# Kernel tuning notes

Hardware: AMD Instinct MI355X
Metric: run time of the kernel (lower is better)

Reference implementation:

```python
import jax, jax.numpy as jnp
import numpy as np

B, S, D, H = 2, 2048, 1024, 16
HD = D // H
SCALE = float(np.sqrt(HD))


def setup_inputs() -> dict:
    key = jax.random.key(0)
    ks = jax.random.split(key, 11)
    std = 1.0 / np.sqrt(D)
    inp = {
        "query": jax.random.normal(ks[0], (B, S, D), dtype=jnp.float32),
        "key": jax.random.normal(ks[1], (B, S, D), dtype=jnp.float32),
        "value": jax.random.normal(ks[2], (B, S, D), dtype=jnp.float32),
        "w_q": jax.random.normal(ks[3], (D, D), dtype=jnp.float32) * std,
        "b_q": jax.random.normal(ks[4], (D,), dtype=jnp.float32) * std,
        "w_k": jax.random.normal(ks[5], (D, D), dtype=jnp.float32) * std,
        "b_k": jax.random.normal(ks[6], (D,), dtype=jnp.float32) * std,
        "w_v": jax.random.normal(ks[7], (D, D), dtype=jnp.float32) * std,
        "b_v": jax.random.normal(ks[8], (D,), dtype=jnp.float32) * std,
        "w_fc": jax.random.normal(ks[9], (D, D), dtype=jnp.float32) * std,
        "b_fc": jax.random.normal(ks[10], (D,), dtype=jnp.float32) * std,
    }
    return inp


def reference(query, key, value, w_q, b_q, w_k, b_k, w_v, b_v, w_fc, b_fc):
    # Linear projections (torch Linear: x @ W^T + b; here w_* stored as [in, out])
    Q = query @ w_q + b_q            # [B, S, D]
    K = key @ w_k + b_k
    V = value @ w_v + b_v
    # split heads -> [B, H, S, HD]
    Q = Q.reshape(B, S, H, HD).transpose(0, 2, 1, 3)
    K = K.reshape(B, S, H, HD).transpose(0, 2, 1, 3)
    V = V.reshape(B, S, H, HD).transpose(0, 2, 1, 3)
    energy = jnp.einsum('bhqd,bhkd->bhqk', Q, K) / SCALE  # [B, H, S, S]
    attn = jax.nn.softmax(energy, axis=-1)
    x = jnp.einsum('bhqk,bhkd->bhqd', attn, V)            # [B, H, S, HD]
    x = x.transpose(0, 2, 1, 3).reshape(B, S, D)
    return x @ w_fc + b_fc
```

## Files before the change

### kernel.cpp

```cpp
#include <hip/hip_runtime.h>
#include <stdint.h>

#define Bz 2
#define Sz 2048
#define Dz 1024
#define Hz 16
#define HDz 64
#define Mz (Bz*Sz)

typedef unsigned short u16;
typedef __attribute__((ext_vector_type(8))) __bf16 bf16x8;
typedef __attribute__((ext_vector_type(8))) unsigned short u16x8;
typedef __attribute__((ext_vector_type(4))) float f32x4;

#define C1 0.1803368801111243f

__device__ __forceinline__ u16 f2bf(float f) {
  union { float f; unsigned u; } v; v.f = f;
  unsigned r = v.u + 0x7fffu + ((v.u >> 16) & 1u);
  return (u16)(r >> 16);
}

__device__ __forceinline__ void async16(void* lds, const void* g) {
  __builtin_amdgcn_global_load_lds(
      (const __attribute__((address_space(1))) unsigned int*)g,
      (__attribute__((address_space(3))) unsigned int*)lds, 16, 0, 0);
}

__global__ void cvt3_kernel(const float* __restrict__ q, const float* __restrict__ k,
                            const float* __restrict__ v,
                            u16* __restrict__ xq, u16* __restrict__ xk, u16* __restrict__ xv,
                            int n4) {
  const float* in = blockIdx.y == 0 ? q : blockIdx.y == 1 ? k : v;
  u16* out = blockIdx.y == 0 ? xq : blockIdx.y == 1 ? xk : xv;
  int i = blockIdx.x * blockDim.x + threadIdx.x;
  if (i < n4) {
    float4 t = ((const float4*)in)[i];
    ((ushort4*)out)[i] = make_ushort4(f2bf(t.x), f2bf(t.y), f2bf(t.z), f2bf(t.w));
  }
}

__global__ void wt_cvt_kernel(const float* __restrict__ w0, const float* __restrict__ w1,
                              const float* __restrict__ w2, const float* __restrict__ w3,
                              u16* __restrict__ Wt ) {
  const float* W = blockIdx.z == 0 ? w0 : blockIdx.z == 1 ? w1 : blockIdx.z == 2 ? w2 : w3;
  u16* o = Wt + (size_t)blockIdx.z * Dz * Dz;
  __shared__ __align__(16) float t[32][33];
  int n0 = blockIdx.x * 32, k0 = blockIdx.y * 32;
  int x = threadIdx.x, y = threadIdx.y;
#pragma unroll
  for (int i = 0; i < 4; ++i)
    t[y + i*8][x] = W[(size_t)(k0 + y + i*8) * Dz + n0 + x];
  __syncthreads();
#pragma unroll
  for (int i = 0; i < 4; ++i)
    o[(size_t)(n0 + y + i*8) * Dz + k0 + x] = f2bf(t[x][y + i*8]);
}

__global__ void __launch_bounds__(256)
vtrans_kernel(const u16* __restrict__ Vp, u16* __restrict__ Vt) {
  __shared__ __align__(16) u16 t[64][72];
  int s0 = blockIdx.x * 64, bh = blockIdx.y;
  int b = bh >> 4;
  int h = bh & 15;
  int tid = threadIdx.x;
#pragma unroll
  for (int p = 0; p < 4; ++p) {
    int c = p * 256 + tid;
    int row = c >> 4, off = (c & 15) * 4;
    ushort4 v = *(const ushort4*)(Vp + (size_t)(b * Sz + s0 + row) * Dz + h * 64 + off);
    *(ushort4*)&t[row][off] = v;
  }
  __syncthreads();
#pragma unroll
  for (int p = 0; p < 4; ++p) {
    int c = p * 256 + tid;
    int d = c >> 4, sc = (c & 15) * 4;
    ushort4 v = make_ushort4(t[sc + 0][d], t[sc + 1][d], t[sc + 2][d], t[sc + 3][d]);
    *(ushort4*)(Vt + (size_t)(bh * 64 + d) * Sz + s0 + sc) = v;
  }
}

__global__ void __launch_bounds__(256)
gemm_qkv(const u16* __restrict__ xq, const u16* __restrict__ xk, const u16* __restrict__ xv,
         const u16* __restrict__ Wt3,
         const float* __restrict__ bq, const float* __restrict__ bk, const float* __restrict__ bv,
         u16* __restrict__ Qp, u16* __restrict__ Kp, u16* __restrict__ Vp)
{
  __shared__ __align__(16) u16 lA[128][32];
  __shared__ __align__(16) u16 lB[128][32];
  const int sel = blockIdx.x >> 3;
  const int n0 = (blockIdx.x & 7) * 128;
  const int m0 = blockIdx.y * 128;
  const u16* A = sel == 0 ? xq : sel == 1 ? xk : xv;
  const u16* Bt = Wt3 + (size_t)sel * Dz * Dz;
  const float* bias = sel == 0 ? bq : sel == 1 ? bk : bv;
  u16* Cv = sel == 0 ? Qp : sel == 1 ? Kp : Vp;

  const int tid = threadIdx.x;
  const int w = tid >> 6, lane = tid & 63;
  const int wm = (w >> 1) * 64, wn = (w & 1) * 64;
  const int l16 = lane & 15, qd = lane >> 4;

  f32x4 acc[4][4];
#pragma unroll
  for (int i = 0; i < 4; ++i)
#pragma unroll
    for (int j = 0; j < 4; ++j) acc[i][j] = (f32x4){0.f, 0.f, 0.f, 0.f};

  const int r0 = tid >> 2, c0 = (tid & 3) * 8;
  const int r1 = r0 + 64;

  for (int k0 = 0; k0 < Dz; k0 += 32) {
    __syncthreads();
    async16(&lA[r0][c0], A  + (size_t)(m0 + r0) * Dz + k0 + c0);
    async16(&lB[r0][c0], Bt + (size_t)(n0 + r0) * Dz + k0 + c0);
    async16(&lA[r1][c0], A  + (size_t)(m0 + r1) * Dz + k0 + c0);
    async16(&lB[r1][c0], Bt + (size_t)(n0 + r1) * Dz + k0 + c0);
    __syncthreads();
    bf16x8 af[4], bfv[4];
#pragma unroll
    for (int t = 0; t < 4; ++t) {
      af[t]  = *(const bf16x8*)&lA[wm + t * 16 + l16][qd * 8];
      bfv[t] = *(const bf16x8*)&lB[wn + t * 16 + l16][qd * 8];
    }
#pragma unroll
    for (int mt = 0; mt < 4; ++mt)
#pragma unroll
      for (int nt = 0; nt < 4; ++nt)
        acc[mt][nt] = __builtin_amdgcn_mfma_f32_16x16x32_bf16(af[mt], bfv[nt], acc[mt][nt], 0, 0, 0);
  }

#pragma unroll
  for (int nt = 0; nt < 4; ++nt) {
    const int n = n0 + wn + nt * 16 + l16;
    const float bvl = bias[n];
#pragma unroll
    for (int mt = 0; mt < 4; ++mt)
#pragma unroll
      for (int r = 0; r < 4; ++r) {
        const int m = m0 + wm + mt * 16 + qd * 4 + r;
        Cv[(size_t)m * Dz + n] = f2bf(acc[mt][nt][r] + bvl);
      }
  }
}

__global__ void __launch_bounds__(256)
gemm_fc(const u16* __restrict__ A, const u16* __restrict__ Bt,
        const float* __restrict__ bias, float* __restrict__ C)
{
  __shared__ __align__(16) u16 lA[128][32];
  __shared__ __align__(16) u16 lB[64][32];
  const int m0 = blockIdx.y * 128, n0 = blockIdx.x * 64;
  const int tid = threadIdx.x;
  const int w = tid >> 6, lane = tid & 63;
  const int wm = (w >> 1) * 64, wn = (w & 1) * 32;
  const int l16 = lane & 15, qd = lane >> 4;

  f32x4 acc[4][2];
#pragma unroll
  for (int i = 0; i < 4; ++i)
#pragma unroll
    for (int j = 0; j < 2; ++j) acc[i][j] = (f32x4){0.f, 0.f, 0.f, 0.f};

  const int r0 = tid >> 2, c0 = (tid & 3) * 8;

  for (int k0 = 0; k0 < Dz; k0 += 32) {
    __syncthreads();
    async16(&lA[r0][c0],      A  + (size_t)(m0 + r0) * Dz + k0 + c0);
    async16(&lA[r0 + 64][c0], A  + (size_t)(m0 + r0 + 64) * Dz + k0 + c0);
    async16(&lB[r0][c0],      Bt + (size_t)(n0 + r0) * Dz + k0 + c0);
    __syncthreads();
    bf16x8 af[4], bfv[2];
#pragma unroll
    for (int t = 0; t < 4; ++t)
      af[t] = *(const bf16x8*)&lA[wm + t * 16 + l16][qd * 8];
#pragma unroll
    for (int t = 0; t < 2; ++t)
      bfv[t] = *(const bf16x8*)&lB[wn + t * 16 + l16][qd * 8];
#pragma unroll
    for (int mt = 0; mt < 4; ++mt)
#pragma unroll
      for (int nt = 0; nt < 2; ++nt)
        acc[mt][nt] = __builtin_amdgcn_mfma_f32_16x16x32_bf16(af[mt], bfv[nt], acc[mt][nt], 0, 0, 0);
  }

#pragma unroll
  for (int nt = 0; nt < 2; ++nt) {
    const int n = n0 + wn + nt * 16 + l16;
    const float bvl = bias[n];
#pragma unroll
    for (int mt = 0; mt < 4; ++mt)
#pragma unroll
      for (int r = 0; r < 4; ++r) {
        const int m = m0 + wm + mt * 16 + qd * 4 + r;
        C[(size_t)m * Dz + n] = acc[mt][nt][r] + bvl;
      }
  }
}

__global__ void __launch_bounds__(256, 2)
attn_kernel(const u16* __restrict__ Qp, const u16* __restrict__ Kp,
            const u16* __restrict__ Vt, u16* __restrict__ Ao)
{
  __shared__ __align__(16) u16 lK[128][72];
  __shared__ __align__(16) u16 lV[64][136];
  __shared__ __align__(16) u16 lP[4][32][136];

  const int q0 = blockIdx.x * 128;
  const int bh = blockIdx.y;
  const int b = bh >> 4, h = bh & 15;
  const int tid = threadIdx.x, w = tid >> 6, lane = tid & 63;
  const int l16 = lane & 15, qd = lane >> 4;

  const int krow = tid >> 3, kcol = (tid & 7) * 8;
  const int vrow = tid >> 4, vcol = (tid & 15) * 8;

  u16x8 kreg[4], vreg[4];
#pragma unroll
  for (int p = 0; p < 4; ++p) {
    kreg[p] = *(const u16x8*)(Kp + (size_t)(b * Sz + p * 32 + krow) * Dz + h * 64 + kcol);
    vreg[p] = *(const u16x8*)(Vt + (size_t)(bh * 64 + p * 16 + vrow) * Sz + vcol);
  }

  bf16x8 qf[2][2];
#pragma unroll
  for (int mt = 0; mt < 2; ++mt)
#pragma unroll
    for (int ks = 0; ks < 2; ++ks)
      qf[mt][ks] = *(const bf16x8*)(Qp + (size_t)(b * Sz + q0 + w * 32 + mt * 16 + l16) * Dz
                                    + h * 64 + ks * 32 + qd * 8);

  u16x8 ob;
#pragma unroll
  for (int i = 0; i < 8; ++i) ob[i] = 0x3F80u;
  const bf16x8 onesf = __builtin_bit_cast(bf16x8, ob);

  f32x4 oacc[2][4], lacc[2];
#pragma unroll
  for (int i = 0; i < 2; ++i) {
    lacc[i] = (f32x4){0.f, 0.f, 0.f, 0.f};
#pragma unroll
    for (int j = 0; j < 4; ++j) oacc[i][j] = (f32x4){0.f, 0.f, 0.f, 0.f};
  }

  for (int t = 0; t < Sz / 128; ++t) {
    __syncthreads();
#pragma unroll
    for (int p = 0; p < 4; ++p) {
      *(u16x8*)&lK[p * 32 + krow][kcol] = kreg[p];
      *(u16x8*)&lV[p * 16 + vrow][vcol] = vreg[p];
    }
    if (t + 1 < Sz / 128) {
      const int kv = (t + 1) * 128;
#pragma unroll
      for (int p = 0; p < 4; ++p) {
        kreg[p] = *(const u16x8*)(Kp + (size_t)(b * Sz + kv + p * 32 + krow) * Dz + h * 64 + kcol);
        vreg[p] = *(const u16x8*)(Vt + (size_t)(bh * 64 + p * 16 + vrow) * Sz + kv + vcol);
      }
    }
    __syncthreads();

    f32x4 sacc[2][8];
#pragma unroll
    for (int i = 0; i < 2; ++i)
#pragma unroll
      for (int j = 0; j < 8; ++j) sacc[i][j] = (f32x4){0.f, 0.f, 0.f, 0.f};
#pragma unroll
    for (int ks = 0; ks < 2; ++ks) {
      bf16x8 bfv[8];
#pragma unroll
      for (int nt = 0; nt < 8; ++nt)
        bfv[nt] = *(const bf16x8*)&lK[nt * 16 + l16][ks * 32 + qd * 8];
#pragma unroll
      for (int mt = 0; mt < 2; ++mt)
#pragma unroll
        for (int nt = 0; nt < 8; ++nt)
          sacc[mt][nt] = __builtin_amdgcn_mfma_f32_16x16x32_bf16(qf[mt][ks], bfv[nt], sacc[mt][nt], 0, 0, 0);
    }

#pragma unroll
    for (int mt = 0; mt < 2; ++mt)
#pragma unroll
      for (int nt = 0; nt < 8; ++nt)
#pragma unroll
        for (int r = 0; r < 4; ++r) {
          float pv = exp2f(sacc[mt][nt][r] * C1);
          unsigned bits = __builtin_bit_cast(unsigned, pv);
          lP[w][mt * 16 + qd * 4 + r][nt * 16 + l16] = (u16)((bits + 0x8000u) >> 16);
        }

#pragma unroll
    for (int ks = 0; ks < 4; ++ks) {
      bf16x8 pa[2], vb[4];
      pa[0] = *(const bf16x8*)&lP[w][l16     ][ks * 32 + qd * 8];
      pa[1] = *(const bf16x8*)&lP[w][16 + l16][ks * 32 + qd * 8];
#pragma unroll
      for (int nt = 0; nt < 4; ++nt)
        vb[nt] = *(const bf16x8*)&lV[nt * 16 + l16][ks * 32 + qd * 8];
#pragma unroll
      for (int mt = 0; mt < 2; ++mt) {
#pragma unroll
        for (int nt = 0; nt < 4; ++nt)
          oacc[mt][nt] = __builtin_amdgcn_mfma_f32_16x16x32_bf16(pa[mt], vb[nt], oacc[mt][nt], 0, 0, 0);
        lacc[mt] = __builtin_amdgcn_mfma_f32_16x16x32_bf16(pa[mt], onesf, lacc[mt], 0, 0, 0);
      }
    }
  }

#pragma unroll
  for (int mt = 0; mt < 2; ++mt)
#pragma unroll
    for (int r = 0; r < 4; ++r) {
      const float inv = 1.0f / lacc[mt][r];
      const int row = q0 + w * 32 + mt * 16 + qd * 4 + r;
#pragma unroll
      for (int nt = 0; nt < 4; ++nt) {
        const int col = h * 64 + nt * 16 + l16;
        Ao[(size_t)(b * Sz + row) * Dz + col] = f2bf(oacc[mt][nt][r] * inv);
      }
    }
}

extern "C" void kernel_launch(void* const* d_in, const int* in_sizes, int n_in,
                              void* d_out, int out_size, void* d_ws, size_t ws_size,
                              hipStream_t stream) {
  const float* query = (const float*)d_in[0];
  const float* key   = (const float*)d_in[1];
  const float* value = (const float*)d_in[2];
  const float* w_q  = (const float*)d_in[3];
  const float* b_q  = (const float*)d_in[4];
  const float* w_k  = (const float*)d_in[5];
  const float* b_k  = (const float*)d_in[6];
  const float* w_v  = (const float*)d_in[7];
  const float* b_v  = (const float*)d_in[8];
  const float* w_fc = (const float*)d_in[9];
  const float* b_fc = (const float*)d_in[10];
  float* out = (float*)d_out;

  const size_t XE = (size_t)Mz * Dz;
  const size_t WE = (size_t)Dz * Dz;
  u16* Xq  = (u16*)d_ws;
  u16* Xk  = Xq + XE;
  u16* Xv  = Xk + XE;
  u16* Wt  = Xv + XE;
  u16* Wtf = Wt + 3 * WE;
  u16* Qp  = Wt + 4 * WE;
  u16* Kp  = Qp + XE;
  u16* Vp  = Kp + XE;
  u16* Vt  = Xk;
  u16* Ao  = Xq;

  const int n4 = (int)(XE / 4);
  cvt3_kernel<<<dim3(n4 / 256, 3), 256, 0, stream>>>(query, key, value, Xq, Xk, Xv, n4);

  wt_cvt_kernel<<<dim3(Dz / 32, Dz / 32, 4), dim3(32, 8), 0, stream>>>(w_q, w_k, w_v, w_fc, Wt);

  gemm_qkv<<<dim3(24, Mz / 128), 256, 0, stream>>>(Xq, Xk, Xv, Wt, b_q, b_k, b_v, Qp, Kp, Vp);

  vtrans_kernel<<<dim3(Sz / 64, Bz * Hz), 256, 0, stream>>>(Vp, Vt);

  attn_kernel<<<dim3(Sz / 128, Bz * Hz), 256, 0, stream>>>(Qp, Kp, Vt, Ao);

  gemm_fc<<<dim3(Dz / 64, Mz / 128), 256, 0, stream>>>(Ao, Wtf, b_fc, out);
}
```

Measured before the change: 252.7 us.

## Rewrite attention as register-only transposed-S flash loop with lane shuffles

The attention kernel no longer stages K, V and P through shared memory. Each wave now computes S^T (K as the A operand) over 32-key tiles, reading K and V fragments straight from global memory with a one-tile K prefetch. It repacks the exponentiated probabilities into an MFMA B operand with cross-lane shuffles, and accumulates row sums in registers rather than with a ones-matrix MFMA. This removes LDS traffic and block barriers, but every wave re-reads K/V from global/L2 with no reuse across the block's four waves, and runs many more loop iterations.

New measurement: 302.9 us. 19.9% more time.

```diff
diff --git a/kernel.cpp b/kernel.cpp
--- a/kernel.cpp
+++ b/kernel.cpp
@@ -19,6 +19,18 @@
   union { float f; unsigned u; } v; v.f = f;
   unsigned r = v.u + 0x7fffu + ((v.u >> 16) & 1u);
   return (u16)(r >> 16);
+}
+
+__device__ __forceinline__ unsigned packbf(float a, float b) {
+  unsigned ua = __builtin_bit_cast(unsigned, a);
+  unsigned ub = __builtin_bit_cast(unsigned, b);
+  return ((ua + 0x8000u) >> 16) | ((ub + 0x8000u) & 0xFFFF0000u);
+}
+
+__device__ __forceinline__ bf16x8 mk8(unsigned a, unsigned b, unsigned c, unsigned d) {
+  union { unsigned u[4]; bf16x8 v; } x;
+  x.u[0] = a; x.u[1] = b; x.u[2] = c; x.u[3] = d;
+  return x.v;
 }
 
 __device__ __forceinline__ void async16(void* lds, const void* g) {
@@ -203,122 +215,125 @@
 attn_kernel(const u16* __restrict__ Qp, const u16* __restrict__ Kp,
             const u16* __restrict__ Vt, u16* __restrict__ Ao)
 {
-  __shared__ __align__(16) u16 lK[128][72];
-  __shared__ __align__(16) u16 lV[64][136];
-  __shared__ __align__(16) u16 lP[4][32][136];
-
   const int q0 = blockIdx.x * 128;
   const int bh = blockIdx.y;
   const int b = bh >> 4, h = bh & 15;
   const int tid = threadIdx.x, w = tid >> 6, lane = tid & 63;
   const int l16 = lane & 15, qd = lane >> 4;
 
-  const int krow = tid >> 3, kcol = (tid & 7) * 8;
-  const int vrow = tid >> 4, vcol = (tid & 15) * 8;
-
-  u16x8 kreg[4], vreg[4];
-#pragma unroll
-  for (int p = 0; p < 4; ++p) {
-    kreg[p] = *(const u16x8*)(Kp + (size_t)(b * Sz + p * 32 + krow) * Dz + h * 64 + kcol);
-    vreg[p] = *(const u16x8*)(Vt + (size_t)(bh * 64 + p * 16 + vrow) * Sz + vcol);
-  }
+  const int   qrow = b * Sz + q0 + w * 32;
+  const int   krow = b * Sz;
+  const size_t hof = (size_t)h * 64;
 
   bf16x8 qf[2][2];
 #pragma unroll
-  for (int mt = 0; mt < 2; ++mt)
-#pragma unroll
-    for (int ks = 0; ks < 2; ++ks)
-      qf[mt][ks] = *(const bf16x8*)(Qp + (size_t)(b * Sz + q0 + w * 32 + mt * 16 + l16) * Dz
-                                    + h * 64 + ks * 32 + qd * 8);
-
-  u16x8 ob;
-#pragma unroll
-  for (int i = 0; i < 8; ++i) ob[i] = 0x3F80u;
-  const bf16x8 onesf = __builtin_bit_cast(bf16x8, ob);
-
-  f32x4 oacc[2][4], lacc[2];
-#pragma unroll
-  for (int i = 0; i < 2; ++i) {
-    lacc[i] = (f32x4){0.f, 0.f, 0.f, 0.f};
-#pragma unroll
-    for (int j = 0; j < 4; ++j) oacc[i][j] = (f32x4){0.f, 0.f, 0.f, 0.f};
-  }
-
-  for (int t = 0; t < Sz / 128; ++t) {
-    __syncthreads();
-#pragma unroll
-    for (int p = 0; p < 4; ++p) {
-      *(u16x8*)&lK[p * 32 + krow][kcol] = kreg[p];
-      *(u16x8*)&lV[p * 16 + vrow][vcol] = vreg[p];
+  for (int qt = 0; qt < 2; ++qt)
+#pragma unroll
+    for (int ksd = 0; ksd < 2; ++ksd)
+      qf[qt][ksd] = *(const bf16x8*)(Qp + (size_t)(qrow + qt * 16 + l16) * Dz + hof + ksd * 32 + qd * 8);
+
+  const int sidx0 = ((qd & 1) * 2) * 16 + l16;
+  const int sidx1 = sidx0 + 16;
+
+  f32x4 oaccT[4][2];
+#pragma unroll
+  for (int mt = 0; mt < 4; ++mt)
+#pragma unroll
+    for (int qt = 0; qt < 2; ++qt) oaccT[mt][qt] = (f32x4){0.f, 0.f, 0.f, 0.f};
+  float lsum[2] = {0.f, 0.f};
+
+  bf16x8 kf[2][2];
+#pragma unroll
+  for (int kvt = 0; kvt < 2; ++kvt)
+#pragma unroll
+    for (int ksd = 0; ksd < 2; ++ksd)
+      kf[kvt][ksd] = *(const bf16x8*)(Kp + (size_t)(krow + kvt * 16 + l16) * Dz + hof + ksd * 32 + qd * 8);
+
+  for (int t = 0; t < Sz / 32; ++t) {
+    const int kv0 = t * 32;
+
+    bf16x8 vf[4];
+#pragma unroll
+    for (int mt = 0; mt < 4; ++mt)
+      vf[mt] = *(const bf16x8*)(Vt + (size_t)(bh * 64 + mt * 16 + l16) * Sz + kv0 + qd * 8);
+
+    const int kvn = ((t + 1) & (Sz / 32 - 1)) * 32;
+    bf16x8 kn[2][2];
+#pragma unroll
+    for (int kvt = 0; kvt < 2; ++kvt)
+#pragma unroll
+      for (int ksd = 0; ksd < 2; ++ksd)
+        kn[kvt][ksd] = *(const bf16x8*)(Kp + (size_t)(krow + kvn + kvt * 16 + l16) * Dz + hof + ksd * 32 + qd * 8);
+
+    f32x4 sacc[2][2];
+#pragma unroll
+    for (int kvt = 0; kvt < 2; ++kvt)
+#pragma unroll
+      for (int qt = 0; qt < 2; ++qt) sacc[kvt][qt] = (f32x4){0.f, 0.f, 0.f, 0.f};
+#pragma unroll
+    for (int ksd = 0; ksd < 2; ++ksd)
+#pragma unroll
+      for (int kvt = 0; kvt < 2; ++kvt)
+#pragma unroll
+        for (int qt = 0; qt < 2; ++qt)
+          sacc[kvt][qt] = __builtin_amdgcn_mfma_f32_16x16x32_bf16(kf[kvt][ksd], qf[qt][ksd], sacc[kvt][qt], 0, 0, 0);
+
+    unsigned pk[2][2][2];
+#pragma unroll
+    for (int kvt = 0; kvt < 2; ++kvt)
+#pragma unroll
+      for (int qt = 0; qt < 2; ++qt) {
+        float e0 = exp2f(sacc[kvt][qt][0] * C1);
+        float e1 = exp2f(sacc[kvt][qt][1] * C1);
+        float e2 = exp2f(sacc[kvt][qt][2] * C1);
+        float e3 = exp2f(sacc[kvt][qt][3] * C1);
+        lsum[qt] += (e0 + e1) + (e2 + e3);
+        pk[kvt][qt][0] = packbf(e0, e1);
+        pk[kvt][qt][1] = packbf(e2, e3);
+      }
+
+#pragma unroll
+    for (int qt = 0; qt < 2; ++qt) {
+      unsigned v[4];
+#pragma unroll
+      for (int i = 0; i < 4; ++i) {
+        const int si = (i >> 1) ? sidx1 : sidx0;
+        unsigned tA = (unsigned)__shfl((int)pk[0][qt][i & 1], si);
+        unsigned tB = (unsigned)__shfl((int)pk[1][qt][i & 1], si);
+        v[i] = (qd & 2) ? tB : tA;
+      }
+      const bf16x8 pb = mk8(v[0], v[1], v[2], v[3]);
+#pragma unroll
+      for (int mt = 0; mt < 4; ++mt)
+        oaccT[mt][qt] = __builtin_amdgcn_mfma_f32_16x16x32_bf16(vf[mt], pb, oaccT[mt][qt], 0, 0, 0);
     }
-    if (t + 1 < Sz / 128) {
-      const int kv = (t + 1) * 128;
-#pragma unroll
-      for (int p = 0; p < 4; ++p) {
-        kreg[p] = *(const u16x8*)(Kp + (size_t)(b * Sz + kv + p * 32 + krow) * Dz + h * 64 + kcol);
-        vreg[p] = *(const u16x8*)(Vt + (size_t)(bh * 64 + p * 16 + vrow) * Sz + kv + vcol);
-      }
-    }
-    __syncthreads();
-
-    f32x4 sacc[2][8];
-#pragma unroll
-    for (int i = 0; i < 2; ++i)
-#pragma unroll
-      for (int j = 0; j < 8; ++j) sacc[i][j] = (f32x4){0.f, 0.f, 0.f, 0.f};
-#pragma unroll
-    for (int ks = 0; ks < 2; ++ks) {
-      bf16x8 bfv[8];
-#pragma unroll
-      for (int nt = 0; nt < 8; ++nt)
-        bfv[nt] = *(const bf16x8*)&lK[nt * 16 + l16][ks * 32 + qd * 8];
-#pragma unroll
-      for (int mt = 0; mt < 2; ++mt)
-#pragma unroll
-        for (int nt = 0; nt < 8; ++nt)
-          sacc[mt][nt] = __builtin_amdgcn_mfma_f32_16x16x32_bf16(qf[mt][ks], bfv[nt], sacc[mt][nt], 0, 0, 0);
-    }
-
-#pragma unroll
-    for (int mt = 0; mt < 2; ++mt)
-#pragma unroll
-      for (int nt = 0; nt < 8; ++nt)
-#pragma unroll
-        for (int r = 0; r < 4; ++r) {
-          float pv = exp2f(sacc[mt][nt][r] * C1);
-          unsigned bits = __builtin_bit_cast(unsigned, pv);
-          lP[w][mt * 16 + qd * 4 + r][nt * 16 + l16] = (u16)((bits + 0x8000u) >> 16);
-        }
-
-#pragma unroll
-    for (int ks = 0; ks < 4; ++ks) {
-      bf16x8 pa[2], vb[4];
-      pa[0] = *(const bf16x8*)&lP[w][l16     ][ks * 32 + qd * 8];
-      pa[1] = *(const bf16x8*)&lP[w][16 + l16][ks * 32 + qd * 8];
-#pragma unroll
-      for (int nt = 0; nt < 4; ++nt)
-        vb[nt] = *(const bf16x8*)&lV[nt * 16 + l16][ks * 32 + qd * 8];
-#pragma unroll
-      for (int mt = 0; mt < 2; ++mt) {
-#pragma unroll
-        for (int nt = 0; nt < 4; ++nt)
-          oacc[mt][nt] = __builtin_amdgcn_mfma_f32_16x16x32_bf16(pa[mt], vb[nt], oacc[mt][nt], 0, 0, 0);
-        lacc[mt] = __builtin_amdgcn_mfma_f32_16x16x32_bf16(pa[mt], onesf, lacc[mt], 0, 0, 0);
-      }
-    }
-  }
-
-#pragma unroll
-  for (int mt = 0; mt < 2; ++mt)
-#pragma unroll
-    for (int r = 0; r < 4; ++r) {
-      const float inv = 1.0f / lacc[mt][r];
-      const int row = q0 + w * 32 + mt * 16 + qd * 4 + r;
-#pragma unroll
-      for (int nt = 0; nt < 4; ++nt) {
-        const int col = h * 64 + nt * 16 + l16;
-        Ao[(size_t)(b * Sz + row) * Dz + col] = f2bf(oacc[mt][nt][r] * inv);
-      }
+
+#pragma unroll
+    for (int kvt = 0; kvt < 2; ++kvt)
+#pragma unroll
+      for (int ksd = 0; ksd < 2; ++ksd)
+        kf[kvt][ksd] = kn[kvt][ksd];
+  }
+
+  float inv[2];
+#pragma unroll
+  for (int qt = 0; qt < 2; ++qt) {
+    float lq = lsum[qt];
+    lq += __shfl_xor(lq, 16);
+    lq += __shfl_xor(lq, 32);
+    inv[qt] = 1.0f / lq;
+  }
+
+#pragma unroll
+  for (int mt = 0; mt < 4; ++mt)
+#pragma unroll
+    for (int qt = 0; qt < 2; ++qt) {
+      const int q = qrow + qt * 16 + l16;
+      ushort4 o = make_ushort4(f2bf(oaccT[mt][qt][0] * inv[qt]),
+                               f2bf(oaccT[mt][qt][1] * inv[qt]),
+                               f2bf(oaccT[mt][qt][2] * inv[qt]),
+                               f2bf(oaccT[mt][qt][3] * inv[qt]));
+      *(ushort4*)(Ao + (size_t)q * Dz + hof + mt * 16 + qd * 4) = o;
     }
 }
 
```
